# Kernel tuning notes

Measured on AMD Instinct MI355X. Metric: run time of the kernel, lower is better.

Reference implementation:

```python
import jax, jax.numpy as jnp
import numpy as np

NUM_EXPERTS = 8
M_TOTAL = 16384      # total routed tokens, sorted by expert
IN_FEATURES = 2048
OUT_FEATURES = 2048


def setup_inputs() -> dict:
    key = jax.random.key(0)
    k1, k2 = jax.random.split(key)
    x = jax.random.normal(k1, (M_TOTAL, IN_FEATURES), dtype=jnp.float32)
    # moe_fused_kaiming_uniform_: uniform(-sqrt(3*5/in), +sqrt(3*5/in))
    bound = float(np.sqrt(3.0 * 5.0 / IN_FEATURES))
    weight = jax.random.uniform(
        k2, (NUM_EXPERTS, OUT_FEATURES, IN_FEATURES),
        dtype=jnp.float32, minval=-bound, maxval=bound)
    # variable-size expert groups that sum exactly to M_TOTAL
    rng = np.random.default_rng(0)
    cuts = np.sort(rng.choice(np.arange(1, M_TOTAL), NUM_EXPERTS - 1, replace=False))
    m_sizes = np.diff(np.concatenate([[0], cuts, [M_TOTAL]])).astype(np.int32)
    return {"input": x, "weight": weight, "m_sizes": jnp.asarray(m_sizes)}


def reference(input, weight, m_sizes):
    """Grouped GEMM: rows of `input` are sorted by expert; the e-th contiguous
    block of m_sizes[e] rows is multiplied by weight[e].T ([out, in] -> x @ W_e^T)."""
    num_experts, out_features, _ = weight.shape
    m = input.shape[0]
    # per-token expert id from group sizes (jit-safe: fixed total length)
    expert_ids = jnp.repeat(jnp.arange(num_experts, dtype=jnp.int32), m_sizes,
                            total_repeat_length=m)  # [M]
    out = jnp.zeros((m, out_features), dtype=input.dtype)
    for e in range(num_experts):  # small fixed expert count
        mask = (expert_ids == e)[:, None]
        out = out + jnp.where(mask, input @ weight[e].T, jnp.zeros((), input.dtype))
    return out
```

## Files before the change

### kernel.cpp

```cpp
#include <hip/hip_runtime.h>
#include <hip/hip_bf16.h>

#define M_TOTAL 16384
#define KDIM 2048
#define NDIM 2048
#define NEXP 8
#define BM 256
#define BN 128
#define BK 32
#define RT_MAX 71
#define CT 16
#define NWG (RT_MAX * CT)
#define BUFB 24576

typedef __attribute__((ext_vector_type(8))) __bf16 bf16x8;
typedef __attribute__((ext_vector_type(4))) float f32x4;

__device__ inline int minI(int a, int b) { return a < b ? a : b; }

__device__ inline bf16x8 cvt8(float4 a, float4 b) {
  bf16x8 r;
  r[0] = (__bf16)a.x; r[1] = (__bf16)a.y; r[2] = (__bf16)a.z; r[3] = (__bf16)a.w;
  r[4] = (__bf16)b.x; r[5] = (__bf16)b.y; r[6] = (__bf16)b.z; r[7] = (__bf16)b.w;
  return r;
}

__device__ inline void gload16(const void* g, void* l) {
  __builtin_amdgcn_global_load_lds(
      (const __attribute__((address_space(1))) void*)g,
      (__attribute__((address_space(3))) void*)l, 16, 0, 0);
}

__global__ __launch_bounds__(256) void cvt_both(
    const float* __restrict__ x, const float* __restrict__ w,
    bf16x8* __restrict__ xb, bf16x8* __restrict__ wb) {
  const int NX = (M_TOTAL * KDIM) / 8;
  const int NW = (NEXP * NDIM * KDIM) / 8;
  const int stride = gridDim.x * blockDim.x;
  for (int i = blockIdx.x * blockDim.x + threadIdx.x; i < NX + NW; i += stride) {
    const float4* src = (i < NX) ? ((const float4*)x + (size_t)i * 2)
                                 : ((const float4*)w + (size_t)(i - NX) * 2);
    float4 a = src[0], b = src[1];
    bf16x8 c = cvt8(a, b);
    if (i < NX) xb[i] = c; else wb[i - NX] = c;
  }
}

__global__ __launch_bounds__(512, 4) void moe_gemm_co(
    const __hip_bfloat16* __restrict__ xb, const __hip_bfloat16* __restrict__ wb,
    const int* __restrict__ ms, float* __restrict__ out) {
  __shared__ __align__(16) char lds[2 * BUFB];

  const int orig = blockIdx.x;
  const int wg = (orig & 7) * (NWG / 8) + (orig >> 3);
  const int bt = wg >> 4;
  const int ntile = wg & 15;

  int sizes[NEXP];
#pragma unroll
  for (int i = 0; i < NEXP; ++i) sizes[i] = ms[i];
  int e = 0, row0 = 0, rows = 0, acc_t = 0, start = 0;
  bool found = false;
#pragma unroll
  for (int i = 0; i < NEXP; ++i) {
    int nt = (sizes[i] + BM - 1) >> 8;
    if (!found && bt < acc_t + nt) {
      found = true; e = i;
      int tt = bt - acc_t;
      row0 = start + tt * BM;
      rows = minI(sizes[i] - tt * BM, BM);
    }
    acc_t += nt; start += sizes[i];
  }
  if (!found) return;

  const int tid = threadIdx.x;
  const int lane = tid & 63;
  const int wave = tid >> 6;
  const int wr = wave >> 1, wc = wave & 1;
  const int col0 = ntile * BN;

  const int rwh = wave * 16 + (lane >> 2);
  const int colel = (((lane & 3) ^ ((lane >> 3) & 3)) << 3);
  const __hip_bfloat16* aS0 = xb + (size_t)minI(row0 + rwh, M_TOTAL - 1) * KDIM + colel;
  const __hip_bfloat16* aS1 = xb + (size_t)minI(row0 + 128 + rwh, M_TOTAL - 1) * KDIM + colel;
  const __hip_bfloat16* wbase = wb + (size_t)e * NDIM * KDIM;
  const __hip_bfloat16* bS = wbase + (size_t)(col0 + rwh) * KDIM + colel;

  const int fr = lane & 15, fc = lane >> 4;
  int offA[4], offB[4];
#pragma unroll
  for (int mt = 0; mt < 4; ++mt) {
    int r = wr * 64 + mt * 16 + fr;
    offA[mt] = r * 64 + ((fc ^ ((r >> 1) & 3)) << 4);
  }
#pragma unroll
  for (int nt = 0; nt < 4; ++nt) {
    int r = wc * 64 + nt * 16 + fr;
    offB[nt] = 16384 + r * 64 + ((fc ^ ((r >> 1) & 3)) << 4);
  }

  f32x4 acc[4][4];
  const f32x4 zero = {0.f, 0.f, 0.f, 0.f};
#pragma unroll
  for (int i = 0; i < 4; ++i)
#pragma unroll
    for (int j = 0; j < 4; ++j) acc[i][j] = zero;

#define ST3(BI, T) { char* b_ = lds + (BI) * BUFB + wave * 1024; \
    gload16(aS0 + (size_t)(T) * BK, b_); \
    gload16(aS1 + (size_t)(T) * BK, b_ + 8192); \
    gload16(bS + (size_t)(T) * BK, b_ + 16384); }

#define TILE(T, BR, BI, DOST) { \
    if (DOST) ST3(BI, (T) + 1); \
    const char* bb_ = lds + (BR) * BUFB; \
    bf16x8 af[4], bv[4]; \
    _Pragma("unroll") for (int mt = 0; mt < 4; ++mt) \
      af[mt] = *(const bf16x8*)(bb_ + offA[mt]); \
    _Pragma("unroll") for (int nt = 0; nt < 4; ++nt) \
      bv[nt] = *(const bf16x8*)(bb_ + offB[nt]); \
    __builtin_amdgcn_s_setprio(1); \
    _Pragma("unroll") for (int nt = 0; nt < 4; ++nt) \
      _Pragma("unroll") for (int mt = 0; mt < 4; ++mt) \
        acc[mt][nt] = __builtin_amdgcn_mfma_f32_16x16x32_bf16( \
            af[mt], bv[nt], acc[mt][nt], 0, 0, 0); \
    __builtin_amdgcn_s_setprio(0); \
    asm volatile("s_waitcnt vmcnt(0)"); \
    __builtin_amdgcn_s_barrier(); \
  }

  ST3(0, 0)
  asm volatile("s_waitcnt vmcnt(0)");
  __builtin_amdgcn_s_barrier();

  for (int i = 0; i < 31; ++i) {
    TILE(2 * i,     0, 1, true)
    TILE(2 * i + 1, 1, 0, true)
  }
  TILE(62, 0, 1, true)
  TILE(63, 1, 0, false)

#undef TILE
#undef ST3

  const int er = (lane >> 4) * 4;
#pragma unroll
  for (int mt = 0; mt < 4; ++mt) {
#pragma unroll
    for (int j = 0; j < 4; ++j) {
      int r = wr * 64 + mt * 16 + er + j;
      if (r < rows) {
        float* op = out + (size_t)(row0 + r) * NDIM + col0 + wc * 64 + (lane & 15);
#pragma unroll
        for (int nt = 0; nt < 4; ++nt) op[nt * 16] = acc[mt][nt][j];
      }
    }
  }
}

__global__ __launch_bounds__(256) void moe_gemm_f32(
    const float* __restrict__ x, const float* __restrict__ w,
    const int* __restrict__ ms, float* __restrict__ out) {
  __shared__ __align__(16) char As[128 * 64 * 2];
  __shared__ __align__(16) char Bs[128 * 64 * 2];
  int sizes[NEXP];
#pragma unroll
  for (int i = 0; i < NEXP; ++i) sizes[i] = ms[i];
  const int bt = blockIdx.y;
  int e = 0, row0 = 0, rows = 0, acc_t = 0, start = 0;
  bool found = false;
#pragma unroll
  for (int i = 0; i < NEXP; ++i) {
    int nt = (sizes[i] + 127) >> 7;
    if (!found && bt < acc_t + nt) {
      found = true; e = i;
      int tt = bt - acc_t;
      row0 = start + tt * 128;
      rows = minI(sizes[i] - tt * 128, 128);
    }
    acc_t += nt; start += sizes[i];
  }
  if (!found) return;
  const int tid = threadIdx.x;
  const int lane = tid & 63;
  const int wave = tid >> 6;
  const int wm = wave >> 1, wn = wave & 1;
  const int col0 = blockIdx.x * 128;
  const float* wbase = w + (size_t)e * (size_t)NDIM * KDIM;
  const int sr = tid >> 1;
  const int sh = tid & 1;
  const float* aptr = x + (size_t)(row0 + sr) * KDIM + sh * 32;
  const float* bptr = wbase + (size_t)(col0 + sr) * KDIM + sh * 32;
  const bool aval = (sr < rows);
  f32x4 acc[4][4];
  const f32x4 zero = {0.f, 0.f, 0.f, 0.f};
#pragma unroll
  for (int i = 0; i < 4; ++i)
#pragma unroll
    for (int j = 0; j < 4; ++j) acc[i][j] = zero;
  for (int kb = 0; kb < KDIM / 64; ++kb) {
    {
      float4 v[8];
      if (aval) {
        const float4* p = (const float4*)(aptr + kb * 64);
#pragma unroll
        for (int j = 0; j < 8; ++j) v[j] = p[j];
      } else {
#pragma unroll
        for (int j = 0; j < 8; ++j) v[j] = make_float4(0.f, 0.f, 0.f, 0.f);
      }
#pragma unroll
      for (int j = 0; j < 4; ++j) {
        bf16x8 c = cvt8(v[2 * j], v[2 * j + 1]);
        int chunk = (sh * 4 + j) ^ (sr & 7);
        *(bf16x8*)(As + sr * 128 + chunk * 16) = c;
      }
    }
    {
      const float4* p = (const float4*)(bptr + kb * 64);
      float4 u[8];
#pragma unroll
      for (int j = 0; j < 8; ++j) u[j] = p[j];
#pragma unroll
      for (int j = 0; j < 4; ++j) {
        bf16x8 c = cvt8(u[2 * j], u[2 * j + 1]);
        int chunk = (sh * 4 + j) ^ (sr & 7);
        *(bf16x8*)(Bs + sr * 128 + chunk * 16) = c;
      }
    }
    __syncthreads();
#pragma unroll
    for (int ks = 0; ks < 2; ++ks) {
      bf16x8 afr[4], bfv[4];
#pragma unroll
      for (int mt = 0; mt < 4; ++mt) {
        int r = wm * 64 + mt * 16 + (lane & 15);
        int chunk = (ks * 4 + (lane >> 4)) ^ (r & 7);
        afr[mt] = *(const bf16x8*)(As + r * 128 + chunk * 16);
      }
#pragma unroll
      for (int nt = 0; nt < 4; ++nt) {
        int r = wn * 64 + nt * 16 + (lane & 15);
        int chunk = (ks * 4 + (lane >> 4)) ^ (r & 7);
        bfv[nt] = *(const bf16x8*)(Bs + r * 128 + chunk * 16);
      }
#pragma unroll
      for (int mt = 0; mt < 4; ++mt)
#pragma unroll
        for (int nt = 0; nt < 4; ++nt)
          acc[mt][nt] = __builtin_amdgcn_mfma_f32_16x16x32_bf16(
              afr[mt], bfv[nt], acc[mt][nt], 0, 0, 0);
    }
    __syncthreads();
  }
#pragma unroll
  for (int mt = 0; mt < 4; ++mt) {
#pragma unroll
    for (int j = 0; j < 4; ++j) {
      int r = wm * 64 + mt * 16 + (lane >> 4) * 4 + j;
      if (r < rows) {
        float* op = out + (size_t)(row0 + r) * NDIM + col0 + wn * 64 + (lane & 15);
#pragma unroll
        for (int nt = 0; nt < 4; ++nt) op[nt * 16] = acc[mt][nt][j];
      }
    }
  }
}

extern "C" void kernel_launch(void* const* d_in, const int* in_sizes, int n_in,
                              void* d_out, int out_size, void* d_ws, size_t ws_size,
                              hipStream_t stream) {
  const float* x = (const float*)d_in[0];
  const float* w = (const float*)d_in[1];
  const int* ms = (const int*)d_in[2];
  float* out = (float*)d_out;
  const size_t nx = (size_t)M_TOTAL * KDIM;
  const size_t nw = (size_t)NEXP * NDIM * KDIM;
  const size_t need = (nx + nw) * sizeof(__hip_bfloat16);
  if (ws_size >= need) {
    __hip_bfloat16* xb = (__hip_bfloat16*)d_ws;
    __hip_bfloat16* wb = xb + nx;
    cvt_both<<<2048, 256, 0, stream>>>(x, w, (bf16x8*)xb, (bf16x8*)wb);
    moe_gemm_co<<<dim3(NWG), dim3(512), 0, stream>>>(xb, wb, ms, out);
  } else {
    moe_gemm_f32<<<dim3(16, 135), dim3(256), 0, stream>>>(x, w, ms, out);
  }
}
```

Baseline: 271.2 us.

## Load B fragments directly to registers and triple-buffer A tiles in LDS

B (weight) fragments now go from global memory straight into registers, double-buffered in two register sets, and no longer pass through LDS. A tiles use a three-stage LDS ring with prefetch distance two, so the wait before each barrier only covers older loads. The aim is to cut LDS traffic and space for B and to hide more global-load latency. In exchange, each B load is a per-lane 16-byte read across strided rows, which may coalesce worse, and the two register sets raise register pressure under the 512x4 launch bound.

```diff
diff --git a/kernel.cpp b/kernel.cpp
--- a/kernel.cpp
+++ b/kernel.cpp
@@ -11,7 +11,7 @@
 #define RT_MAX 71
 #define CT 16
 #define NWG (RT_MAX * CT)
-#define BUFB 24576
+#define ABUF 16384
 
 typedef __attribute__((ext_vector_type(8))) __bf16 bf16x8;
 typedef __attribute__((ext_vector_type(4))) float f32x4;
@@ -46,10 +46,10 @@
   }
 }
 
-__global__ __launch_bounds__(512, 4) void moe_gemm_co(
+__global__ __launch_bounds__(512, 4) void moe_gemm_bg(
     const __hip_bfloat16* __restrict__ xb, const __hip_bfloat16* __restrict__ wb,
     const int* __restrict__ ms, float* __restrict__ out) {
-  __shared__ __align__(16) char lds[2 * BUFB];
+  __shared__ __align__(16) char lds[3 * ABUF];
 
   const int orig = blockIdx.x;
   const int wg = (orig & 7) * (NWG / 8) + (orig >> 3);
@@ -84,21 +84,20 @@
   const int colel = (((lane & 3) ^ ((lane >> 3) & 3)) << 3);
   const __hip_bfloat16* aS0 = xb + (size_t)minI(row0 + rwh, M_TOTAL - 1) * KDIM + colel;
   const __hip_bfloat16* aS1 = xb + (size_t)minI(row0 + 128 + rwh, M_TOTAL - 1) * KDIM + colel;
+
+  const int fr = lane & 15, fc = lane >> 4;
   const __hip_bfloat16* wbase = wb + (size_t)e * NDIM * KDIM;
-  const __hip_bfloat16* bS = wbase + (size_t)(col0 + rwh) * KDIM + colel;
-
-  const int fr = lane & 15, fc = lane >> 4;
-  int offA[4], offB[4];
+  const __hip_bfloat16* bG0 = wbase + (size_t)(col0 + wc * 64 +  0 + fr) * KDIM + fc * 8;
+  const __hip_bfloat16* bG1 = wbase + (size_t)(col0 + wc * 64 + 16 + fr) * KDIM + fc * 8;
+  const __hip_bfloat16* bG2 = wbase + (size_t)(col0 + wc * 64 + 32 + fr) * KDIM + fc * 8;
+  const __hip_bfloat16* bG3 = wbase + (size_t)(col0 + wc * 64 + 48 + fr) * KDIM + fc * 8;
+
+  int offA[4];
 #pragma unroll
   for (int mt = 0; mt < 4; ++mt) {
     int r = wr * 64 + mt * 16 + fr;
     offA[mt] = r * 64 + ((fc ^ ((r >> 1) & 3)) << 4);
   }
-#pragma unroll
-  for (int nt = 0; nt < 4; ++nt) {
-    int r = wc * 64 + nt * 16 + fr;
-    offB[nt] = 16384 + r * 64 + ((fc ^ ((r >> 1) & 3)) << 4);
-  }
 
   f32x4 acc[4][4];
   const f32x4 zero = {0.f, 0.f, 0.f, 0.f};
@@ -107,42 +106,57 @@
 #pragma unroll
     for (int j = 0; j < 4; ++j) acc[i][j] = zero;
 
-#define ST3(BI, T) { char* b_ = lds + (BI) * BUFB + wave * 1024; \
+  bf16x8 bvX[4], bvY[4];
+
+#define ST2(BI, T) { char* b_ = lds + (BI) * ABUF + wave * 1024; \
     gload16(aS0 + (size_t)(T) * BK, b_); \
-    gload16(aS1 + (size_t)(T) * BK, b_ + 8192); \
-    gload16(bS + (size_t)(T) * BK, b_ + 16384); }
-
-#define TILE(T, BR, BI, DOST) { \
-    if (DOST) ST3(BI, (T) + 1); \
-    const char* bb_ = lds + (BR) * BUFB; \
-    bf16x8 af[4], bv[4]; \
+    gload16(aS1 + (size_t)(T) * BK, b_ + 8192); }
+#define LDB(SET, T) { \
+    bv##SET[0] = *(const bf16x8*)(bG0 + (T) * 32); \
+    bv##SET[1] = *(const bf16x8*)(bG1 + (T) * 32); \
+    bv##SET[2] = *(const bf16x8*)(bG2 + (T) * 32); \
+    bv##SET[3] = *(const bf16x8*)(bG3 + (T) * 32); }
+
+#define TILE(T, BR, BI2, CUR, NXT, DOB, DOA, VM) { \
+    if (DOB) LDB(NXT, (T) + 1); \
+    if (DOA) ST2(BI2, (T) + 2); \
+    const char* bb_ = lds + (BR) * ABUF; \
+    bf16x8 af[4]; \
     _Pragma("unroll") for (int mt = 0; mt < 4; ++mt) \
       af[mt] = *(const bf16x8*)(bb_ + offA[mt]); \
-    _Pragma("unroll") for (int nt = 0; nt < 4; ++nt) \
-      bv[nt] = *(const bf16x8*)(bb_ + offB[nt]); \
     __builtin_amdgcn_s_setprio(1); \
     _Pragma("unroll") for (int nt = 0; nt < 4; ++nt) \
       _Pragma("unroll") for (int mt = 0; mt < 4; ++mt) \
         acc[mt][nt] = __builtin_amdgcn_mfma_f32_16x16x32_bf16( \
-            af[mt], bv[nt], acc[mt][nt], 0, 0, 0); \
+            af[mt], bv##CUR[nt], acc[mt][nt], 0, 0, 0); \
     __builtin_amdgcn_s_setprio(0); \
-    asm volatile("s_waitcnt vmcnt(0)"); \
+    asm volatile("s_waitcnt " VM); \
     __builtin_amdgcn_s_barrier(); \
   }
 
-  ST3(0, 0)
-  asm volatile("s_waitcnt vmcnt(0)");
+  ST2(0, 0)
+  ST2(1, 1)
+  LDB(X, 0)
+  asm volatile("s_waitcnt vmcnt(6)");
   __builtin_amdgcn_s_barrier();
 
-  for (int i = 0; i < 31; ++i) {
-    TILE(2 * i,     0, 1, true)
-    TILE(2 * i + 1, 1, 0, true)
-  }
-  TILE(62, 0, 1, true)
-  TILE(63, 1, 0, false)
+  for (int i = 0; i < 10; ++i) {
+    const int t = 6 * i;
+    TILE(t,     0, 2, X, Y, true, true, "vmcnt(6)")
+    TILE(t + 1, 1, 0, Y, X, true, true, "vmcnt(6)")
+    TILE(t + 2, 2, 1, X, Y, true, true, "vmcnt(6)")
+    TILE(t + 3, 0, 2, Y, X, true, true, "vmcnt(6)")
+    TILE(t + 4, 1, 0, X, Y, true, true, "vmcnt(6)")
+    TILE(t + 5, 2, 1, Y, X, true, true, "vmcnt(6)")
+  }
+  TILE(60, 0, 2, X, Y, true,  true,  "vmcnt(6)")
+  TILE(61, 1, 0, Y, X, true,  true,  "vmcnt(6)")
+  TILE(62, 2, 0, X, Y, true,  false, "vmcnt(4)")
+  TILE(63, 0, 0, Y, X, false, false, "vmcnt(0)")
 
 #undef TILE
-#undef ST3
+#undef LDB
+#undef ST2
 
   const int er = (lane >> 4) * 4;
 #pragma unroll
@@ -282,7 +296,7 @@
     __hip_bfloat16* xb = (__hip_bfloat16*)d_ws;
     __hip_bfloat16* wb = xb + nx;
     cvt_both<<<2048, 256, 0, stream>>>(x, w, (bf16x8*)xb, (bf16x8*)wb);
-    moe_gemm_co<<<dim3(NWG), dim3(512), 0, stream>>>(xb, wb, ms, out);
+    moe_gemm_bg<<<dim3(NWG), dim3(512), 0, stream>>>(xb, wb, ms, out);
   } else {
     moe_gemm_f32<<<dim3(16, 135), dim3(256), 0, stream>>>(x, w, ms, out);
   }
```

Result: slower. 890.9 us (+228.5%).

## Prepack operands into MFMA fragment order and read directly from global memory

Applied to the files above, without the earlier changes.

The conversion kernel now writes bf16 operands in a per-tile, per-lane fragment layout, padding A tiles by expert group. The GEMM drops LDS staging, async global-to-LDS loads and barriers, and each wave loads its MFMA fragments straight from global memory with coalesced 16-byte reads. This removes LDS traffic and synchronisation but loses the shared reuse inside the workgroup, relies on cache for the duplicated reads across waves, and exposes global load latency. Launch bounds now target 2 workgroups per CU.

```diff
diff --git a/kernel.cpp b/kernel.cpp
--- a/kernel.cpp
+++ b/kernel.cpp
@@ -7,11 +7,11 @@
 #define NEXP 8
 #define BM 256
 #define BN 128
-#define BK 32
 #define RT_MAX 71
 #define CT 16
 #define NWG (RT_MAX * CT)
-#define BUFB 24576
+#define A_UNITS (RT_MAX * 16 * 64 * 64)
+#define W_UNITS (NEXP * 128 * 64 * 64)
 
 typedef __attribute__((ext_vector_type(8))) __bf16 bf16x8;
 typedef __attribute__((ext_vector_type(4))) float f32x4;
@@ -25,32 +25,51 @@
   return r;
 }
 
-__device__ inline void gload16(const void* g, void* l) {
-  __builtin_amdgcn_global_load_lds(
-      (const __attribute__((address_space(1))) void*)g,
-      (__attribute__((address_space(3))) void*)l, 16, 0, 0);
-}
-
-__global__ __launch_bounds__(256) void cvt_both(
+__global__ __launch_bounds__(256) void pack_ops(
     const float* __restrict__ x, const float* __restrict__ w,
-    bf16x8* __restrict__ xb, bf16x8* __restrict__ wb) {
-  const int NX = (M_TOTAL * KDIM) / 8;
-  const int NW = (NEXP * NDIM * KDIM) / 8;
+    const int* __restrict__ ms, bf16x8* __restrict__ xp, bf16x8* __restrict__ wp) {
+  const int total = A_UNITS + W_UNITS;
   const int stride = gridDim.x * blockDim.x;
-  for (int i = blockIdx.x * blockDim.x + threadIdx.x; i < NX + NW; i += stride) {
-    const float4* src = (i < NX) ? ((const float4*)x + (size_t)i * 2)
-                                 : ((const float4*)w + (size_t)(i - NX) * 2);
-    float4 a = src[0], b = src[1];
-    bf16x8 c = cvt8(a, b);
-    if (i < NX) xb[i] = c; else wb[i - NX] = c;
-  }
-}
-
-__global__ __launch_bounds__(512, 4) void moe_gemm_co(
-    const __hip_bfloat16* __restrict__ xb, const __hip_bfloat16* __restrict__ wb,
+  for (int i = blockIdx.x * blockDim.x + threadIdx.x; i < total; i += stride) {
+    if (i < A_UNITS) {
+      const int l = i & 63;
+      const int t = (i >> 6) & 63;
+      const int m16 = (i >> 12) & 15;
+      const int bt = i >> 16;
+      int row0 = 0, acc_t = 0, start = 0;
+      bool found = false;
+#pragma unroll
+      for (int q = 0; q < NEXP; ++q) {
+        int sz = ms[q];
+        int nt = (sz + BM - 1) >> 8;
+        if (!found && bt < acc_t + nt) {
+          found = true;
+          row0 = start + (bt - acc_t) * BM;
+        }
+        acc_t += nt; start += sz;
+      }
+      if (!found) continue;
+      const int row = minI(row0 + m16 * 16 + (l & 15), M_TOTAL - 1);
+      const int k = t * 32 + (l >> 4) * 8;
+      const float4* s = (const float4*)(x + (size_t)row * KDIM + k);
+      xp[i] = cvt8(s[0], s[1]);
+    } else {
+      const int v = i - A_UNITS;
+      const int l = v & 63;
+      const int t = (v >> 6) & 63;
+      const int c16 = (v >> 12) & 127;
+      const int e = v >> 19;
+      const int col = c16 * 16 + (l & 15);
+      const int k = t * 32 + (l >> 4) * 8;
+      const float4* s = (const float4*)(w + ((size_t)e * NDIM + col) * KDIM + k);
+      wp[v] = cvt8(s[0], s[1]);
+    }
+  }
+}
+
+__global__ __launch_bounds__(512, 2) void moe_gemm_st(
+    const __hip_bfloat16* __restrict__ xp, const __hip_bfloat16* __restrict__ wp,
     const int* __restrict__ ms, float* __restrict__ out) {
-  __shared__ __align__(16) char lds[2 * BUFB];
-
   const int orig = blockIdx.x;
   const int wg = (orig & 7) * (NWG / 8) + (orig >> 3);
   const int bt = wg >> 4;
@@ -80,25 +99,10 @@
   const int wr = wave >> 1, wc = wave & 1;
   const int col0 = ntile * BN;
 
-  const int rwh = wave * 16 + (lane >> 2);
-  const int colel = (((lane & 3) ^ ((lane >> 3) & 3)) << 3);
-  const __hip_bfloat16* aS0 = xb + (size_t)minI(row0 + rwh, M_TOTAL - 1) * KDIM + colel;
-  const __hip_bfloat16* aS1 = xb + (size_t)minI(row0 + 128 + rwh, M_TOTAL - 1) * KDIM + colel;
-  const __hip_bfloat16* wbase = wb + (size_t)e * NDIM * KDIM;
-  const __hip_bfloat16* bS = wbase + (size_t)(col0 + rwh) * KDIM + colel;
-
-  const int fr = lane & 15, fc = lane >> 4;
-  int offA[4], offB[4];
-#pragma unroll
-  for (int mt = 0; mt < 4; ++mt) {
-    int r = wr * 64 + mt * 16 + fr;
-    offA[mt] = r * 64 + ((fc ^ ((r >> 1) & 3)) << 4);
-  }
-#pragma unroll
-  for (int nt = 0; nt < 4; ++nt) {
-    int r = wc * 64 + nt * 16 + fr;
-    offB[nt] = 16384 + r * 64 + ((fc ^ ((r >> 1) & 3)) << 4);
-  }
+  const char* aB = (const char*)xp + ((size_t)bt << 20) +
+                   (size_t)(wr * 4) * 65536 + lane * 16;
+  const char* bB = (const char*)wp + ((size_t)e << 23) +
+                   (size_t)(ntile * 8 + wc * 4) * 65536 + lane * 16;
 
   f32x4 acc[4][4];
   const f32x4 zero = {0.f, 0.f, 0.f, 0.f};
@@ -107,42 +111,22 @@
 #pragma unroll
     for (int j = 0; j < 4; ++j) acc[i][j] = zero;
 
-#define ST3(BI, T) { char* b_ = lds + (BI) * BUFB + wave * 1024; \
-    gload16(aS0 + (size_t)(T) * BK, b_); \
-    gload16(aS1 + (size_t)(T) * BK, b_ + 8192); \
-    gload16(bS + (size_t)(T) * BK, b_ + 16384); }
-
-#define TILE(T, BR, BI, DOST) { \
-    if (DOST) ST3(BI, (T) + 1); \
-    const char* bb_ = lds + (BR) * BUFB; \
-    bf16x8 af[4], bv[4]; \
-    _Pragma("unroll") for (int mt = 0; mt < 4; ++mt) \
-      af[mt] = *(const bf16x8*)(bb_ + offA[mt]); \
-    _Pragma("unroll") for (int nt = 0; nt < 4; ++nt) \
-      bv[nt] = *(const bf16x8*)(bb_ + offB[nt]); \
-    __builtin_amdgcn_s_setprio(1); \
-    _Pragma("unroll") for (int nt = 0; nt < 4; ++nt) \
-      _Pragma("unroll") for (int mt = 0; mt < 4; ++mt) \
-        acc[mt][nt] = __builtin_amdgcn_mfma_f32_16x16x32_bf16( \
-            af[mt], bv[nt], acc[mt][nt], 0, 0, 0); \
-    __builtin_amdgcn_s_setprio(0); \
-    asm volatile("s_waitcnt vmcnt(0)"); \
-    __builtin_amdgcn_s_barrier(); \
-  }
-
-  ST3(0, 0)
-  asm volatile("s_waitcnt vmcnt(0)");
-  __builtin_amdgcn_s_barrier();
-
-  for (int i = 0; i < 31; ++i) {
-    TILE(2 * i,     0, 1, true)
-    TILE(2 * i + 1, 1, 0, true)
-  }
-  TILE(62, 0, 1, true)
-  TILE(63, 1, 0, false)
-
-#undef TILE
-#undef ST3
+#pragma unroll 4
+  for (int t = 0; t < 64; ++t) {
+    bf16x8 af[4], bv[4];
+#pragma unroll
+    for (int mt = 0; mt < 4; ++mt)
+      af[mt] = *(const bf16x8*)(aB + mt * 65536 + t * 1024);
+#pragma unroll
+    for (int nt = 0; nt < 4; ++nt)
+      bv[nt] = *(const bf16x8*)(bB + nt * 65536 + t * 1024);
+#pragma unroll
+    for (int nt = 0; nt < 4; ++nt)
+#pragma unroll
+      for (int mt = 0; mt < 4; ++mt)
+        acc[mt][nt] = __builtin_amdgcn_mfma_f32_16x16x32_bf16(
+            af[mt], bv[nt], acc[mt][nt], 0, 0, 0);
+  }
 
   const int er = (lane >> 4) * 4;
 #pragma unroll
@@ -275,14 +259,13 @@
   const float* w = (const float*)d_in[1];
   const int* ms = (const int*)d_in[2];
   float* out = (float*)d_out;
-  const size_t nx = (size_t)M_TOTAL * KDIM;
-  const size_t nw = (size_t)NEXP * NDIM * KDIM;
-  const size_t need = (nx + nw) * sizeof(__hip_bfloat16);
+  const size_t need = ((size_t)A_UNITS + W_UNITS) * 16;
   if (ws_size >= need) {
-    __hip_bfloat16* xb = (__hip_bfloat16*)d_ws;
-    __hip_bfloat16* wb = xb + nx;
-    cvt_both<<<2048, 256, 0, stream>>>(x, w, (bf16x8*)xb, (bf16x8*)wb);
-    moe_gemm_co<<<dim3(NWG), dim3(512), 0, stream>>>(xb, wb, ms, out);
+    bf16x8* xp = (bf16x8*)d_ws;
+    bf16x8* wp = xp + A_UNITS;
+    pack_ops<<<4096, 256, 0, stream>>>(x, w, ms, xp, wp);
+    moe_gemm_st<<<dim3(NWG), dim3(512), 0, stream>>>(
+        (const __hip_bfloat16*)xp, (const __hip_bfloat16*)wp, ms, out);
   } else {
     moe_gemm_f32<<<dim3(16, 135), dim3(256), 0, stream>>>(x, w, ms, out);
   }
```

After: 298.1 us. 1.1x slower.
